# Performance work log

Hardware: AMD Instinct MI355X
Metric: run time of the kernel (lower is better)

## Reference

```python
import jax, jax.numpy as jnp
import numpy as np

K = 7            # involution kernel size
GC = 16          # group_channels (canonical involution)
EPS = 1e-6


def ln_cf(x, w, b):
    # channels_first LayerNorm over channel dim (axis=1), as in ConvNeXt utils
    u = jnp.mean(x, axis=1, keepdims=True)
    s = jnp.mean((x - u) ** 2, axis=1, keepdims=True)
    xn = (x - u) / jnp.sqrt(s + EPS)
    return w[:, None, None] * xn + b[:, None, None]


def gelu(x):
    return jax.nn.gelu(x, approximate=False)  # torch nn.GELU default (erf)


def involution(x, w1, b1, w2, b2):
    # x: (B,C,H,W). Kernel-generating head: 1x1 conv -> ReLU -> 1x1 conv.
    B, C, H, W = x.shape
    G = C // GC
    mid = jnp.einsum('bchw,mc->bmhw', x, w1) + b1[None, :, None, None]
    mid = jax.nn.relu(mid)
    wk = jnp.einsum('bmhw,km->bkhw', mid, w2) + b2[None, :, None, None]
    wk = wk.reshape(B, G, K * K, H, W)  # per-pixel, per-group K*K kernels
    pad = (K - 1) // 2
    xp = jnp.pad(x, ((0, 0), (0, 0), (pad, pad), (pad, pad)))
    out = jnp.zeros((B, G, GC, H, W), dtype=x.dtype)
    # accumulate over the K*K spatial offsets (fixed small loop, no big unfold)
    for idx in range(K * K):
        i, j = divmod(idx, K)
        xs = xp[:, :, i:i + H, j:j + W].reshape(B, G, GC, H, W)
        out = out + wk[:, :, idx][:, :, None] * xs
    return out.reshape(B, C, H, W)


def setup_inputs() -> dict:
    key = jax.random.key(0)
    ks = jax.random.split(key, 8)
    B, C, O, H, Wd = 4, 128, 256, 128, 128
    mid = C // 4
    G = C // GC
    sc = 0.05
    return {
        'x': jax.random.normal(ks[0], (B, C, H, Wd), jnp.float32),
        'w1': jax.random.normal(ks[1], (mid, C), jnp.float32) * sc,
        'b1': jnp.zeros((mid,), jnp.float32),
        'w2': jax.random.normal(ks[2], (K * K * G, mid), jnp.float32) * sc,
        'b2': jnp.zeros((K * K * G,), jnp.float32),
        'ln1_w': jnp.ones((C,), jnp.float32),
        'ln1_b': jnp.zeros((C,), jnp.float32),
        'conv_w': jax.random.normal(ks[3], (O, C), jnp.float32) * sc,
        'ln2_w': jnp.ones((O,), jnp.float32),
        'ln2_b': jnp.zeros((O,), jnp.float32),
        'map_w': jax.random.normal(ks[4], (O, C), jnp.float32) * sc,
        'map_b': jnp.zeros((O,), jnp.float32),
        'ln3_w': jnp.ones((O,), jnp.float32),
        'ln3_b': jnp.zeros((O,), jnp.float32),
    }


def reference(x, w1, b1, w2, b2, ln1_w, ln1_b, conv_w, ln2_w, ln2_b,
              map_w, map_b, ln3_w, ln3_b):
    # invblock: Involution -> LayerNorm(channels_first) -> GELU
    x1 = involution(x, w1, b1, w2, b2)
    x1 = gelu(ln_cf(x1, ln1_w, ln1_b))
    # conv_block: 1x1 conv (no bias) -> LayerNorm
    x1 = ln_cf(jnp.einsum('bchw,oc->bohw', x1, conv_w), ln2_w, ln2_b)
    # mapping (channels differ): 1x1 conv (bias) -> LayerNorm
    xm = jnp.einsum('bchw,oc->bohw', x, map_w) + map_b[None, :, None, None]
    xm = ln_cf(xm, ln3_w, ln3_b)
    return gelu(x1 + xm)
```

## Files before the change

kernel.cpp:

```cpp
#include <hip/hip_runtime.h>

typedef unsigned short ushort_t;
typedef unsigned int uint_t;

#define NB 4
#define NC 128
#define NH 128
#define NW 128
#define NPIX 65536
#define NMID 32
#define NKK 49
#define NK 392
#define NKP 400
#define NO 256
#define LN_EPS 1e-6f

typedef __attribute__((ext_vector_type(8))) short short8;
typedef __attribute__((ext_vector_type(4))) float floatx4;

__device__ __forceinline__ float bf2f(ushort_t u) {
    union { uint_t i; float f; } v; v.i = ((uint_t)u) << 16; return v.f;
}
__device__ __forceinline__ float bf2f_lo(uint_t u) {
    union { uint_t i; float f; } v; v.i = u << 16; return v.f;
}
__device__ __forceinline__ float bf2f_hi(uint_t u) {
    union { uint_t i; float f; } v; v.i = u & 0xffff0000u; return v.f;
}
__device__ __forceinline__ ushort_t f2bf(float f) {
    union { float f; uint_t i; } v; v.f = f;
    uint_t x = v.i;
    uint_t r = (x + 0x7FFFu + ((x >> 16) & 1u)) >> 16;
    return (ushort_t)r;
}
__device__ __forceinline__ float gelu_f(float x) {
    return 0.5f * x * (1.0f + erff(x * 0.70710678118654752f));
}
__device__ __forceinline__ float ldin(const void* p, int i, int isf32) {
    return isf32 ? ((const float*)p)[i] : bf2f(((const ushort_t*)p)[i]);
}
__device__ __forceinline__ void gload_lds16(const void* g, void* l) {
    __builtin_amdgcn_global_load_lds(
        (const __attribute__((address_space(1))) void*)g,
        (__attribute__((address_space(3))) void*)l, 16, 0, 0);
}

__global__ void kdetect(const uint_t* __restrict__ xw, int* __restrict__ flag) {
    int lane = threadIdx.x;
    int cnt = 0;
    for (int j = 0; j < 8; j++) {
        uint_t w = xw[lane * 8 + j];
        uint_t e = (w >> 7) & 0xffu;
        if (e >= 110u && e <= 135u) cnt++;
    }
    for (int d = 1; d < 64; d <<= 1) cnt += __shfl_xor(cnt, d);
    if (lane == 0) flag[0] = (cnt < 256) ? 1 : 0;
}

__global__ void ksentinel(uint_t* __restrict__ out, int nwords) {
    int i = blockIdx.x * 256 + threadIdx.x;
    if (i < nwords) out[i] = 0x40004000u;
}

__global__ __launch_bounds__(256) void ktrans(const void* __restrict__ x,
                                              ushort_t* __restrict__ xT,
                                              const int* __restrict__ flag) {
    int isf32 = flag[0];
    int b = blockIdx.z, h = blockIdx.y;
    int wchunk = blockIdx.x & 1, cchunk = blockIdx.x >> 1;
    int w0 = wchunk << 6, c0 = cchunk << 5;
    __shared__ ushort_t tile[32][66];
    int tx = threadIdx.x & 63, ty = threadIdx.x >> 6;
    for (int r = 0; r < 32; r += 4) {
        int idx = (((b * NC + c0 + r + ty) * NH) + h) * NW + w0 + tx;
        tile[r + ty][tx] = isf32 ? f2bf(((const float*)x)[idx])
                                 : ((const ushort_t*)x)[idx];
    }
    __syncthreads();
    int cc = threadIdx.x & 31, wq = threadIdx.x >> 5;
    for (int pp = 0; pp < 64; pp += 8) {
        int wx = pp + wq;
        xT[((size_t)((b * NH + h) * NW) + w0 + wx) * NC + c0 + cc] = tile[cc][wx];
    }
}

__global__ __launch_bounds__(256) void kprep(const void* w1, const void* w2,
                                             const void* b1, const void* b2,
                                             const void* ln1w, const void* ln1b,
                                             const void* ln2w, const void* ln2b,
                                             const void* map_b,
                                             const void* ln3w, const void* ln3b,
                                             const int* __restrict__ flag,
                                             ushort_t* __restrict__ w1b,
                                             ushort_t* __restrict__ w2b,
                                             float* __restrict__ b1f,
                                             float* __restrict__ b2f,
                                             float* __restrict__ ln1wf,
                                             float* __restrict__ ln1bf,
                                             float* __restrict__ ln2wf,
                                             float* __restrict__ ln2bf,
                                             float* __restrict__ mbf,
                                             float* __restrict__ ln3wf,
                                             float* __restrict__ ln3bf) {
    int isf32 = flag[0];
    int i = blockIdx.x * 256 + threadIdx.x;
    if (i < NMID * NC) w1b[i] = f2bf(ldin(w1, i, isf32));
    if (i < NKP * NMID) w2b[i] = (i < NK * NMID) ? f2bf(ldin(w2, i, isf32))
                                                 : (ushort_t)0;
    if (i < NMID) b1f[i] = ldin(b1, i, isf32);
    if (i < NKP)  b2f[i] = (i < NK) ? ldin(b2, i, isf32) : 0.f;
    if (i < NC) { ln1wf[i] = ldin(ln1w, i, isf32); ln1bf[i] = ldin(ln1b, i, isf32); }
    if (i < NO) {
        ln2wf[i] = ldin(ln2w, i, isf32); ln2bf[i] = ldin(ln2b, i, isf32);
        mbf[i]   = ldin(map_b, i, isf32);
        ln3wf[i] = ldin(ln3w, i, isf32); ln3bf[i] = ldin(ln3b, i, isf32);
    }
}

__global__ __launch_bounds__(256) void kfrag(const void* conv_w, const void* map_w,
                                             const int* __restrict__ flag,
                                             ushort_t* __restrict__ wfrag) {
    int isf32 = flag[0];
    int cid = blockIdx.x * 256 + threadIdx.x;
    int lane = cid & 63, n4 = (cid >> 6) & 15, br = (cid >> 10) & 1, kb = cid >> 11;
    int o = n4 * 16 + (lane & 15);
    int ch0 = kb * 32 + (lane >> 4) * 8;
    const void* src = br ? map_w : conv_w;
    ushort_t* dst = wfrag + (size_t)cid * 8;
#pragma unroll
    for (int j = 0; j < 8; j++)
        dst[j] = f2bf(ldin(src, o * NC + ch0 + j, isf32));
}

__global__ __launch_bounds__(256) void k1a(const ushort_t* __restrict__ xT,
                                           const ushort_t* __restrict__ w1b,
                                           const float* __restrict__ b1f,
                                           const ushort_t* __restrict__ w2b,
                                           const float* __restrict__ b2f,
                                           ushort_t* __restrict__ wkT) {
    __shared__ ushort_t midbuf[64 * 32];
    __shared__ ushort_t wkstage[NKP * 66];

    int t = threadIdx.x;
    int lane = t & 63;
    int w = __builtin_amdgcn_readfirstlane(t >> 6);
    int l16 = lane & 15, quad = lane >> 4;
    int tileid = blockIdx.x;
    int tilex = tileid & 15, tiley = (tileid >> 4) & 15, b = tileid >> 8;
    int h0 = tiley * 8, w0 = tilex * 8;

    int lpx_a = 16 * w + l16;
    int py = lpx_a >> 3, pxx = lpx_a & 7;
    const ushort_t* abase = xT + (size_t)((b * NH + h0 + py) * NW + w0 + pxx) * NC + quad * 8;
    floatx4 am0 = (floatx4)0.f, am1 = (floatx4)0.f;
#pragma unroll
    for (int kb = 0; kb < 4; kb++) {
        short8 a   = *(const short8*)(abase + kb * 32);
        short8 b0  = *(const short8*)(w1b + (l16) * NC + kb * 32 + quad * 8);
        short8 b1v = *(const short8*)(w1b + (16 + l16) * NC + kb * 32 + quad * 8);
        am0 = __builtin_amdgcn_mfma_f32_16x16x32_bf16(a, b0, am0, 0, 0, 0);
        am1 = __builtin_amdgcn_mfma_f32_16x16x32_bf16(a, b1v, am1, 0, 0, 0);
    }
    {
        float bia0 = b1f[l16], bia1 = b1f[16 + l16];
#pragma unroll
        for (int r = 0; r < 4; r++) {
            int m = 16 * w + quad * 4 + r;
            midbuf[m * 32 + l16]      = f2bf(fmaxf(am0[r] + bia0, 0.f));
            midbuf[m * 32 + 16 + l16] = f2bf(fmaxf(am1[r] + bia1, 0.f));
        }
    }
    __syncthreads();

    short8 aM = *(const short8*)(midbuf + (16 * w + l16) * 32 + quad * 8);
#pragma unroll
    for (int nt = 0; nt < 25; nt++) {
        int n = nt * 16 + l16;
        short8 bw = *(const short8*)(w2b + n * 32 + quad * 8);
        floatx4 c = __builtin_amdgcn_mfma_f32_16x16x32_bf16(aM, bw, (floatx4)0.f, 0, 0, 0);
        float bias = b2f[n];
#pragma unroll
        for (int r = 0; r < 4; r++)
            wkstage[n * 66 + 16 * w + quad * 4 + r] = f2bf(c[r] + bias);
    }
    __syncthreads();

    int krow = t >> 5, px2 = t & 31;
    for (int it = 0; it < 50; it++) {
        int k = it * 8 + krow;
        uint_t v = *(const uint_t*)&wkstage[k * 66 + 2 * px2];
        *(uint_t*)&wkT[(size_t)k * NPIX + tileid * 64 + 2 * px2] = v;
    }
}

__global__ __launch_bounds__(512) void k1b(const ushort_t* __restrict__ xT,
                                           const ushort_t* __restrict__ wkT,
                                           const float* __restrict__ ln1wf,
                                           const float* __restrict__ ln1bf,
                                           ushort_t* __restrict__ y1) {
    __shared__ __align__(16) char smem[50432];
    uint4* x8   = (uint4*)smem;
    float* sred = (float*)smem;

    int t = threadIdx.x;
    int lane = t & 63;
    int w = __builtin_amdgcn_readfirstlane(t >> 6);
    int tileid = blockIdx.x;
    int tilex = tileid & 15, tiley = (tileid >> 4) & 15, b = tileid >> 8;
    int h0 = tiley * 8, w0 = tilex * 8;
    int py = lane >> 3, pxx = lane & 7;

    const ushort_t* wkbase = wkT + (size_t)(w * NKK) * NPIX + tileid * 64 + lane;
    uint_t wkp[25];
#pragma unroll
    for (int j = 0; j < 24; j++) {
        uint_t lo = wkbase[(size_t)(2 * j) * NPIX];
        uint_t hi = wkbase[(size_t)(2 * j + 1) * NPIX];
        wkp[j] = lo | (hi << 16);
    }
    wkp[24] = wkbase[(size_t)48 * NPIX];

    for (int it = 0; it < 7; it++) {
        int idx = it * 512 + t;
        if (idx < 3136) {
            int oct = idx & 15, hp = idx >> 4;
            int hy = hp / 14, hx = hp - hy * 14;
            int gh = h0 + hy - 3, gw = w0 + hx - 3;
            uint4 v = make_uint4(0u, 0u, 0u, 0u);
            if ((unsigned)gh < (unsigned)NH && (unsigned)gw < (unsigned)NW) {
                v = *(const uint4*)&xT[(size_t)((b * NH + gh) * NW + gw) * NC + 8 * oct];
            }
            x8[oct * 197 + hp] = v;
        }
    }
    __syncthreads();

    int base0 = py * 14 + pxx;
    float a[16];
#pragma unroll
    for (int j = 0; j < 16; j++) a[j] = 0.f;

#pragma unroll
    for (int tap = 0; tap < NKK; tap++) {
        float wkf = (tap & 1) ? bf2f((ushort_t)(wkp[tap >> 1] >> 16))
                              : bf2f((ushort_t)(wkp[tap >> 1] & 0xffffu));
        int xa = base0 + (tap / 7) * 14 + (tap % 7);
        uint4 u0 = x8[(2 * w) * 197 + xa];
        uint4 u1 = x8[(2 * w + 1) * 197 + xa];
        a[0]  = fmaf(wkf, bf2f_lo(u0.x), a[0]);
        a[1]  = fmaf(wkf, bf2f_hi(u0.x), a[1]);
        a[2]  = fmaf(wkf, bf2f_lo(u0.y), a[2]);
        a[3]  = fmaf(wkf, bf2f_hi(u0.y), a[3]);
        a[4]  = fmaf(wkf, bf2f_lo(u0.z), a[4]);
        a[5]  = fmaf(wkf, bf2f_hi(u0.z), a[5]);
        a[6]  = fmaf(wkf, bf2f_lo(u0.w), a[6]);
        a[7]  = fmaf(wkf, bf2f_hi(u0.w), a[7]);
        a[8]  = fmaf(wkf, bf2f_lo(u1.x), a[8]);
        a[9]  = fmaf(wkf, bf2f_hi(u1.x), a[9]);
        a[10] = fmaf(wkf, bf2f_lo(u1.y), a[10]);
        a[11] = fmaf(wkf, bf2f_hi(u1.y), a[11]);
        a[12] = fmaf(wkf, bf2f_lo(u1.z), a[12]);
        a[13] = fmaf(wkf, bf2f_hi(u1.z), a[13]);
        a[14] = fmaf(wkf, bf2f_lo(u1.w), a[14]);
        a[15] = fmaf(wkf, bf2f_hi(u1.w), a[15]);
    }
    __syncthreads();

    float s = 0.f, sq = 0.f;
#pragma unroll
    for (int j = 0; j < 16; j++) { s += a[j]; sq += a[j] * a[j]; }
    sred[(w * 64 + lane) * 2]     = s;
    sred[(w * 64 + lane) * 2 + 1] = sq;
    __syncthreads();
    float ts = 0.f, tq = 0.f;
#pragma unroll
    for (int r = 0; r < 8; r++) {
        ts += sred[(r * 64 + lane) * 2];
        tq += sred[(r * 64 + lane) * 2 + 1];
    }
    float mean = ts * (1.0f / NC);
    float var = tq * (1.0f / NC) - mean * mean;
    float rstd = rsqrtf(var + LN_EPS);

    int p = (b * NH + h0 + py) * NW + w0 + pxx;
    uint_t pk[8];
#pragma unroll
    for (int j = 0; j < 8; j++) {
        int c0 = 16 * w + 2 * j;
        float g0 = gelu_f((a[2 * j] - mean) * rstd * ln1wf[c0] + ln1bf[c0]);
        float g1 = gelu_f((a[2 * j + 1] - mean) * rstd * ln1wf[c0 + 1] + ln1bf[c0 + 1]);
        pk[j] = (uint_t)f2bf(g0) | ((uint_t)f2bf(g1) << 16);
    }
    uint4* dst = (uint4*)(y1 + (size_t)p * NC + 16 * w);
    dst[0] = make_uint4(pk[0], pk[1], pk[2], pk[3]);
    dst[1] = make_uint4(pk[4], pk[5], pk[6], pk[7]);
}

__global__ __launch_bounds__(64) void k1_fused(const ushort_t* __restrict__ xT,
                                               const ushort_t* __restrict__ w1b,
                                               const float* __restrict__ b1f,
                                               const ushort_t* __restrict__ w2b,
                                               const float* __restrict__ b2f,
                                               const float* __restrict__ ln1wf,
                                               const float* __restrict__ ln1bf,
                                               ushort_t* __restrict__ y1) {
    __shared__ ushort_t midbuf[16 * 32];
    __shared__ ushort_t wkbuf[16 * NKP];

    int lane = threadIdx.x;
    int l16 = lane & 15, quad = lane >> 4;
    int b = blockIdx.z;
    int h0 = blockIdx.y * 2, w0 = blockIdx.x * 8;

    int Pa = (b * NH + h0 + (l16 >> 3)) * NW + w0 + (l16 & 7);
    const ushort_t* abase = xT + (size_t)Pa * NC + quad * 8;
    floatx4 am0 = (floatx4)0.f, am1 = (floatx4)0.f;
#pragma unroll
    for (int kb = 0; kb < 4; kb++) {
        short8 a   = *(const short8*)(abase + kb * 32);
        short8 b0  = *(const short8*)(w1b + (l16) * NC + kb * 32 + quad * 8);
        short8 b1v = *(const short8*)(w1b + (16 + l16) * NC + kb * 32 + quad * 8);
        am0 = __builtin_amdgcn_mfma_f32_16x16x32_bf16(a, b0, am0, 0, 0, 0);
        am1 = __builtin_amdgcn_mfma_f32_16x16x32_bf16(a, b1v, am1, 0, 0, 0);
    }
    {
        float bia0 = b1f[l16], bia1 = b1f[16 + l16];
#pragma unroll
        for (int r = 0; r < 4; r++) {
            int m = quad * 4 + r;
            midbuf[m * 32 + l16]      = f2bf(fmaxf(am0[r] + bia0, 0.f));
            midbuf[m * 32 + 16 + l16] = f2bf(fmaxf(am1[r] + bia1, 0.f));
        }
    }
    __syncthreads();

    short8 aM = *(const short8*)(midbuf + l16 * 32 + quad * 8);
#pragma unroll
    for (int nt = 0; nt < 25; nt++) {
        int n = nt * 16 + l16;
        short8 bw = *(const short8*)(w2b + n * 32 + quad * 8);
        floatx4 c = __builtin_amdgcn_mfma_f32_16x16x32_bf16(aM, bw, (floatx4)0.f, 0, 0, 0);
        float bias = b2f[n];
#pragma unroll
        for (int r = 0; r < 4; r++)
            wkbuf[(quad * 4 + r) * NKP + n] = f2bf(c[r] + bias);
    }
    __syncthreads();

    int g = lane >> 3;
    float l1w0 = ln1wf[2 * lane], l1w1 = ln1wf[2 * lane + 1];
    float l1b0 = ln1bf[2 * lane], l1b1 = ln1bf[2 * lane + 1];

    for (int i = 0; i < 16; i++) {
        int hh0 = h0 + (i >> 3), ww0 = w0 + (i & 7);
        int p = (b * NH + hh0) * NW + ww0;
        const ushort_t* wkrow = wkbuf + i * NKP + g * NKK;
        float a0 = 0.f, a1 = 0.f;
#pragma unroll
        for (int dy = -3; dy <= 3; dy++) {
            int hh = hh0 + dy;
            if ((unsigned)hh >= (unsigned)NH) continue;
#pragma unroll
            for (int dx = -3; dx <= 3; dx++) {
                int ww = ww0 + dx;
                if ((unsigned)ww >= (unsigned)NW) continue;
                float wkv = bf2f(wkrow[(dy + 3) * 7 + (dx + 3)]);
                uint_t xp = *(const uint_t*)(xT + ((size_t)(p + dy * NW + dx)) * NC + 2 * lane);
                a0 = fmaf(wkv, bf2f((ushort_t)(xp & 0xffffu)), a0);
                a1 = fmaf(wkv, bf2f((ushort_t)(xp >> 16)), a1);
            }
        }
        float s = a0 + a1, sq = a0 * a0 + a1 * a1;
#pragma unroll
        for (int d = 1; d < 64; d <<= 1) {
            s  += __shfl_xor(s, d);
            sq += __shfl_xor(sq, d);
        }
        float mean = s * (1.0f / NC);
        float var = sq * (1.0f / NC) - mean * mean;
        float rstd = rsqrtf(var + LN_EPS);
        float g0 = gelu_f((a0 - mean) * rstd * l1w0 + l1b0);
        float g1 = gelu_f((a1 - mean) * rstd * l1w1 + l1b1);
        uint_t pk = (uint_t)f2bf(g0) | ((uint_t)f2bf(g1) << 16);
        *(uint_t*)(y1 + (size_t)p * NC + 2 * lane) = pk;
    }
}

__global__ __launch_bounds__(256, 4) void k23(const ushort_t* __restrict__ y1,
                                              const ushort_t* __restrict__ xT,
                                              const ushort_t* __restrict__ wfrag,
                                              const float* __restrict__ mbf,
                                              const float* __restrict__ ln2wf,
                                              const float* __restrict__ ln2bf,
                                              const float* __restrict__ ln3wf,
                                              const float* __restrict__ ln3bf,
                                              void* __restrict__ out,
                                              const int* __restrict__ flag) {
    __shared__ __align__(16) char sbuf[32768];

    int isf32 = flag[0];
    int t = threadIdx.x;
    int lane = t & 63;
    int w = __builtin_amdgcn_readfirstlane(t >> 6);
    int quad = lane >> 4, l16 = lane & 15;
    int pair = w >> 1;
    int oh   = w & 1;

    int P0 = blockIdx.x * 32;
    int pw = P0 + pair * 16;
    const ushort_t* aYp = y1 + (size_t)(pw + l16) * NC + quad * 8;
    const ushort_t* aXp = xT + (size_t)(pw + l16) * NC + quad * 8;

    {
        const ushort_t* gsrc = wfrag + (size_t)(w * 512 + lane) * 8;
        char* ldst = sbuf + (size_t)(w * 512) * 16;
#pragma unroll
        for (int i = 0; i < 8; i++)
            gload_lds16(gsrc + i * 64 * 8, ldst + i * 64 * 16);
    }
    short8 Ay[4], Ax[4];
#pragma unroll
    for (int kb = 0; kb < 4; kb++) {
        Ay[kb] = *(const short8*)(aYp + kb * 32);
        Ax[kb] = *(const short8*)(aXp + kb * 32);
    }
    __syncthreads();

    floatx4 accC[8], accM[8];
#pragma unroll
    for (int j = 0; j < 8; j++) { accC[j] = (floatx4)0.f; accM[j] = (floatx4)0.f; }

#pragma unroll
    for (int kb = 0; kb < 4; kb++) {
        short8 ay = Ay[kb], ax = Ax[kb];
#pragma unroll
        for (int j = 0; j < 8; j++) {
            int n4 = oh * 8 + j;
            short8 bc = *(const short8*)(sbuf + (size_t)(n4 * 64 + lane) * 16);
            short8 bm = *(const short8*)(sbuf + 16384 + (size_t)(n4 * 64 + lane) * 16);
            accC[j] = __builtin_amdgcn_mfma_f32_16x16x32_bf16(ay, bc, accC[j], 0, 0, 0);
            accM[j] = __builtin_amdgcn_mfma_f32_16x16x32_bf16(ax, bm, accM[j], 0, 0, 0);
        }
        __syncthreads();
        if (kb < 3) {
            const ushort_t* gsrc = wfrag + ((size_t)(kb + 1) * 2048 + w * 512 + lane) * 8;
            char* ldst = sbuf + (size_t)(w * 512) * 16;
#pragma unroll
            for (int i = 0; i < 8; i++)
                gload_lds16(gsrc + i * 64 * 8, ldst + i * 64 * 16);
            __syncthreads();
        }
    }

#pragma unroll
    for (int j = 0; j < 8; j++) {
        float mb = mbf[(oh * 8 + j) * 16 + l16];
#pragma unroll
        for (int r = 0; r < 4; r++) accM[j][r] += mb;
    }

    floatx4 s1 = (floatx4)0.f, q1 = (floatx4)0.f, s2 = (floatx4)0.f, q2 = (floatx4)0.f;
#pragma unroll
    for (int j = 0; j < 8; j++)
#pragma unroll
        for (int r = 0; r < 4; r++) {
            float a = accC[j][r], m = accM[j][r];
            s1[r] += a; q1[r] += a * a;
            s2[r] += m; q2[r] += m * m;
        }
#pragma unroll
    for (int d = 1; d < 16; d <<= 1) {
#pragma unroll
        for (int r = 0; r < 4; r++) {
            s1[r] += __shfl_xor(s1[r], d);
            q1[r] += __shfl_xor(q1[r], d);
            s2[r] += __shfl_xor(s2[r], d);
            q2[r] += __shfl_xor(q2[r], d);
        }
    }

    float* sstat = (float*)sbuf;
    if (l16 == 0) {
#pragma unroll
        for (int r = 0; r < 4; r++) {
            float* sp = sstat + (((pair * 2 + oh) * 16) + quad * 4 + r) * 4;
            sp[0] = s1[r]; sp[1] = q1[r]; sp[2] = s2[r]; sp[3] = q2[r];
        }
    }
    __syncthreads();

    floatx4 mn1, rs1, mn2, rs2;
#pragma unroll
    for (int r = 0; r < 4; r++) {
        const float* op = sstat + (((pair * 2 + (oh ^ 1)) * 16) + quad * 4 + r) * 4;
        float S1 = s1[r] + op[0], Q1 = q1[r] + op[1];
        float S2 = s2[r] + op[2], Q2 = q2[r] + op[3];
        mn1[r] = S1 * (1.0f / NO);
        rs1[r] = rsqrtf(Q1 * (1.0f / NO) - mn1[r] * mn1[r] + LN_EPS);
        mn2[r] = S2 * (1.0f / NO);
        rs2[r] = rsqrtf(Q2 * (1.0f / NO) - mn2[r] * mn2[r] + LN_EPS);
    }

    int batch = pw >> 14;
    int plocal = (pw & 16383) + quad * 4;
#pragma unroll
    for (int j = 0; j < 8; j++) {
        int o = (oh * 8 + j) * 16 + l16;
        float l2w = ln2wf[o], l2b = ln2bf[o];
        float l3w = ln3wf[o], l3b = ln3bf[o];
        float4 gv;
        {
            float v1, v2;
            v1 = (accC[j][0] - mn1[0]) * rs1[0] * l2w + l2b;
            v2 = (accM[j][0] - mn2[0]) * rs2[0] * l3w + l3b;
            gv.x = gelu_f(v1 + v2);
            v1 = (accC[j][1] - mn1[1]) * rs1[1] * l2w + l2b;
            v2 = (accM[j][1] - mn2[1]) * rs2[1] * l3w + l3b;
            gv.y = gelu_f(v1 + v2);
            v1 = (accC[j][2] - mn1[2]) * rs1[2] * l2w + l2b;
            v2 = (accM[j][2] - mn2[2]) * rs2[2] * l3w + l3b;
            gv.z = gelu_f(v1 + v2);
            v1 = (accC[j][3] - mn1[3]) * rs1[3] * l2w + l2b;
            v2 = (accM[j][3] - mn2[3]) * rs2[3] * l3w + l3b;
            gv.w = gelu_f(v1 + v2);
        }
        size_t oi = ((size_t)(batch * NO + o) << 14) + plocal;
        if (isf32) {
            *(float4*)((float*)out + oi) = gv;
        } else {
            uint_t p0 = (uint_t)f2bf(gv.x) | ((uint_t)f2bf(gv.y) << 16);
            uint_t p1 = (uint_t)f2bf(gv.z) | ((uint_t)f2bf(gv.w) << 16);
            *(uint2*)((ushort_t*)out + oi) = make_uint2(p0, p1);
        }
    }
}

extern "C" void kernel_launch(void* const* d_in, const int* in_sizes, int n_in,
                              void* d_out, int out_size, void* d_ws, size_t ws_size,
                              hipStream_t stream) {
    const void* x      = d_in[0];
    const void* w1     = d_in[1];
    const void* b1     = d_in[2];
    const void* w2     = d_in[3];
    const void* b2     = d_in[4];
    const void* ln1w   = d_in[5];
    const void* ln1b   = d_in[6];
    const void* conv_w = d_in[7];
    const void* ln2w   = d_in[8];
    const void* ln2b   = d_in[9];
    const void* map_w  = d_in[10];
    const void* map_b  = d_in[11];
    const void* ln3w   = d_in[12];
    const void* ln3b   = d_in[13];

    char* ws = (char*)d_ws;
    ushort_t* xT    = (ushort_t*)(ws);
    ushort_t* y1    = (ushort_t*)(ws + 16777216);
    ushort_t* wfrag = (ushort_t*)(ws + 33554432);
    ushort_t* w1b   = (ushort_t*)(ws + 33685504);
    ushort_t* w2b   = (ushort_t*)(ws + 33693696);
    float*    b1f   = (float*)(ws + 33719296);
    float*    b2f   = (float*)(ws + 33719424);
    float*    ln1wf = (float*)(ws + 33721024);
    float*    ln1bf = (float*)(ws + 33721536);
    float*    mbf   = (float*)(ws + 33722048);
    float*    ln2wf = (float*)(ws + 33723072);
    float*    ln2bf = (float*)(ws + 33724096);
    float*    ln3wf = (float*)(ws + 33725120);
    float*    ln3bf = (float*)(ws + 33726144);
    int*      flag  = (int*)(ws + 33727168);
    const size_t NEED_SMALL = 33727184;
    ushort_t* wkT   = (ushort_t*)(ws + 33727232);
    const size_t NEED_BIG = 33727232 + (size_t)NKP * NPIX * 2;

    if (ws_size < NEED_SMALL) {
        int nwords = out_size / 2;
        ksentinel<<<(nwords + 255) / 256, 256, 0, stream>>>((uint_t*)d_out, nwords);
        return;
    }

    kdetect<<<1, 64, 0, stream>>>((const uint_t*)x, flag);
    kprep<<<128, 256, 0, stream>>>(w1, w2, b1, b2, ln1w, ln1b,
                                   ln2w, ln2b, map_b, ln3w, ln3b, flag,
                                   w1b, w2b, b1f, b2f, ln1wf, ln1bf,
                                   ln2wf, ln2bf, mbf, ln3wf, ln3bf);
    kfrag<<<32, 256, 0, stream>>>(conv_w, map_w, flag, wfrag);
    ktrans<<<dim3(8, 128, 4), 256, 0, stream>>>(x, xT, flag);

    if (ws_size >= NEED_BIG) {
        k1a<<<1024, 256, 0, stream>>>(xT, w1b, b1f, w2b, b2f, wkT);
        k1b<<<1024, 512, 0, stream>>>(xT, wkT, ln1wf, ln1bf, y1);
    } else {
        k1_fused<<<dim3(16, 64, 4), 64, 0, stream>>>(xT, w1b, b1f, w2b, b2f,
                                                     ln1wf, ln1bf, y1);
    }

    k23<<<NPIX / 32, 256, 0, stream>>>(y1, xT, wfrag, mbf,
                                       ln2wf, ln2bf, ln3wf, ln3bf, d_out, flag);
}
```

Baseline: 222.9 us.

## Fuse kernel generation and involution into one kernel, merge prep launches

Merges the per-pixel kernel-generating head (k1a) and the involution+LayerNorm+GELU stage (k1b) into a single 512-thread kernel that keeps the generated 7x7 weights in shared memory. This removes the large wkT round trip through global memory. The weight-prep and fragment-packing kernels are also combined into one launch. The involution now reads x neighbours straight from global memory instead of from a staged shared-memory halo, so it relies on cache reuse, and the channel reduction uses an 8-lane shuffle.

New measurement: 223.5 us. Within noise of the previous version (+0.3%).

```diff
diff --git a/kernel.cpp b/kernel.cpp
--- a/kernel.cpp
+++ b/kernel.cpp
@@ -84,60 +84,62 @@
     }
 }
 
-__global__ __launch_bounds__(256) void kprep(const void* w1, const void* w2,
-                                             const void* b1, const void* b2,
-                                             const void* ln1w, const void* ln1b,
-                                             const void* ln2w, const void* ln2b,
-                                             const void* map_b,
-                                             const void* ln3w, const void* ln3b,
-                                             const int* __restrict__ flag,
-                                             ushort_t* __restrict__ w1b,
-                                             ushort_t* __restrict__ w2b,
-                                             float* __restrict__ b1f,
-                                             float* __restrict__ b2f,
-                                             float* __restrict__ ln1wf,
-                                             float* __restrict__ ln1bf,
-                                             float* __restrict__ ln2wf,
-                                             float* __restrict__ ln2bf,
-                                             float* __restrict__ mbf,
-                                             float* __restrict__ ln3wf,
-                                             float* __restrict__ ln3bf) {
+__global__ __launch_bounds__(256) void kprepfrag(const void* w1, const void* w2,
+                                                 const void* b1, const void* b2,
+                                                 const void* ln1w, const void* ln1b,
+                                                 const void* ln2w, const void* ln2b,
+                                                 const void* map_b,
+                                                 const void* ln3w, const void* ln3b,
+                                                 const void* conv_w, const void* map_w,
+                                                 const int* __restrict__ flag,
+                                                 ushort_t* __restrict__ w1b,
+                                                 ushort_t* __restrict__ w2b,
+                                                 float* __restrict__ b1f,
+                                                 float* __restrict__ b2f,
+                                                 float* __restrict__ ln1wf,
+                                                 float* __restrict__ ln1bf,
+                                                 float* __restrict__ ln2wf,
+                                                 float* __restrict__ ln2bf,
+                                                 float* __restrict__ mbf,
+                                                 float* __restrict__ ln3wf,
+                                                 float* __restrict__ ln3bf,
+                                                 ushort_t* __restrict__ wfrag) {
     int isf32 = flag[0];
-    int i = blockIdx.x * 256 + threadIdx.x;
-    if (i < NMID * NC) w1b[i] = f2bf(ldin(w1, i, isf32));
-    if (i < NKP * NMID) w2b[i] = (i < NK * NMID) ? f2bf(ldin(w2, i, isf32))
-                                                 : (ushort_t)0;
-    if (i < NMID) b1f[i] = ldin(b1, i, isf32);
-    if (i < NKP)  b2f[i] = (i < NK) ? ldin(b2, i, isf32) : 0.f;
-    if (i < NC) { ln1wf[i] = ldin(ln1w, i, isf32); ln1bf[i] = ldin(ln1b, i, isf32); }
-    if (i < NO) {
-        ln2wf[i] = ldin(ln2w, i, isf32); ln2bf[i] = ldin(ln2b, i, isf32);
-        mbf[i]   = ldin(map_b, i, isf32);
-        ln3wf[i] = ldin(ln3w, i, isf32); ln3bf[i] = ldin(ln3b, i, isf32);
-    }
-}
-
-__global__ __launch_bounds__(256) void kfrag(const void* conv_w, const void* map_w,
-                                             const int* __restrict__ flag,
-                                             ushort_t* __restrict__ wfrag) {
-    int isf32 = flag[0];
-    int cid = blockIdx.x * 256 + threadIdx.x;
-    int lane = cid & 63, n4 = (cid >> 6) & 15, br = (cid >> 10) & 1, kb = cid >> 11;
-    int o = n4 * 16 + (lane & 15);
-    int ch0 = kb * 32 + (lane >> 4) * 8;
-    const void* src = br ? map_w : conv_w;
-    ushort_t* dst = wfrag + (size_t)cid * 8;
-#pragma unroll
-    for (int j = 0; j < 8; j++)
-        dst[j] = f2bf(ldin(src, o * NC + ch0 + j, isf32));
-}
-
-__global__ __launch_bounds__(256) void k1a(const ushort_t* __restrict__ xT,
+    int bid = blockIdx.x;
+    if (bid < 128) {
+        int i = bid * 256 + threadIdx.x;
+        if (i < NMID * NC) w1b[i] = f2bf(ldin(w1, i, isf32));
+        if (i < NKP * NMID) w2b[i] = (i < NK * NMID) ? f2bf(ldin(w2, i, isf32))
+                                                     : (ushort_t)0;
+        if (i < NMID) b1f[i] = ldin(b1, i, isf32);
+        if (i < NKP)  b2f[i] = (i < NK) ? ldin(b2, i, isf32) : 0.f;
+        if (i < NC) { ln1wf[i] = ldin(ln1w, i, isf32); ln1bf[i] = ldin(ln1b, i, isf32); }
+        if (i < NO) {
+            ln2wf[i] = ldin(ln2w, i, isf32); ln2bf[i] = ldin(ln2b, i, isf32);
+            mbf[i]   = ldin(map_b, i, isf32);
+            ln3wf[i] = ldin(ln3w, i, isf32); ln3bf[i] = ldin(ln3b, i, isf32);
+        }
+    } else {
+        int cid = (bid - 128) * 256 + threadIdx.x;
+        int lane = cid & 63, n4 = (cid >> 6) & 15, br = (cid >> 10) & 1, kb = cid >> 11;
+        int o = n4 * 16 + (lane & 15);
+        int ch0 = kb * 32 + (lane >> 4) * 8;
+        const void* src = br ? map_w : conv_w;
+        ushort_t* dst = wfrag + (size_t)cid * 8;
+#pragma unroll
+        for (int j = 0; j < 8; j++)
+            dst[j] = f2bf(ldin(src, o * NC + ch0 + j, isf32));
+    }
+}
+
+__global__ __launch_bounds__(512) void k1f(const ushort_t* __restrict__ xT,
                                            const ushort_t* __restrict__ w1b,
                                            const float* __restrict__ b1f,
                                            const ushort_t* __restrict__ w2b,
                                            const float* __restrict__ b2f,
-                                           ushort_t* __restrict__ wkT) {
+                                           const float* __restrict__ ln1wf,
+                                           const float* __restrict__ ln1bf,
+                                           ushort_t* __restrict__ y1) {
     __shared__ ushort_t midbuf[64 * 32];
     __shared__ ushort_t wkstage[NKP * 66];
 
@@ -148,20 +150,21 @@
     int tileid = blockIdx.x;
     int tilex = tileid & 15, tiley = (tileid >> 4) & 15, b = tileid >> 8;
     int h0 = tiley * 8, w0 = tilex * 8;
-
-    int lpx_a = 16 * w + l16;
-    int py = lpx_a >> 3, pxx = lpx_a & 7;
-    const ushort_t* abase = xT + (size_t)((b * NH + h0 + py) * NW + w0 + pxx) * NC + quad * 8;
-    floatx4 am0 = (floatx4)0.f, am1 = (floatx4)0.f;
-#pragma unroll
-    for (int kb = 0; kb < 4; kb++) {
-        short8 a   = *(const short8*)(abase + kb * 32);
-        short8 b0  = *(const short8*)(w1b + (l16) * NC + kb * 32 + quad * 8);
-        short8 b1v = *(const short8*)(w1b + (16 + l16) * NC + kb * 32 + quad * 8);
-        am0 = __builtin_amdgcn_mfma_f32_16x16x32_bf16(a, b0, am0, 0, 0, 0);
-        am1 = __builtin_amdgcn_mfma_f32_16x16x32_bf16(a, b1v, am1, 0, 0, 0);
-    }
-    {
+    int w4 = w & 3;
+
+    if (w < 4) {
+        int lpx = 16 * w + l16;
+        int py = lpx >> 3, pxx = lpx & 7;
+        const ushort_t* abase = xT + (size_t)((b * NH + h0 + py) * NW + w0 + pxx) * NC + quad * 8;
+        floatx4 am0 = (floatx4)0.f, am1 = (floatx4)0.f;
+#pragma unroll
+        for (int kb = 0; kb < 4; kb++) {
+            short8 a   = *(const short8*)(abase + kb * 32);
+            short8 b0  = *(const short8*)(w1b + (l16) * NC + kb * 32 + quad * 8);
+            short8 b1v = *(const short8*)(w1b + (16 + l16) * NC + kb * 32 + quad * 8);
+            am0 = __builtin_amdgcn_mfma_f32_16x16x32_bf16(a, b0, am0, 0, 0, 0);
+            am1 = __builtin_amdgcn_mfma_f32_16x16x32_bf16(a, b1v, am1, 0, 0, 0);
+        }
         float bia0 = b1f[l16], bia1 = b1f[16 + l16];
 #pragma unroll
         for (int r = 0; r < 4; r++) {
@@ -172,218 +175,86 @@
     }
     __syncthreads();
 
-    short8 aM = *(const short8*)(midbuf + (16 * w + l16) * 32 + quad * 8);
-#pragma unroll
-    for (int nt = 0; nt < 25; nt++) {
-        int n = nt * 16 + l16;
-        short8 bw = *(const short8*)(w2b + n * 32 + quad * 8);
-        floatx4 c = __builtin_amdgcn_mfma_f32_16x16x32_bf16(aM, bw, (floatx4)0.f, 0, 0, 0);
-        float bias = b2f[n];
-#pragma unroll
-        for (int r = 0; r < 4; r++)
-            wkstage[n * 66 + 16 * w + quad * 4 + r] = f2bf(c[r] + bias);
+    {
+        short8 aM = *(const short8*)(midbuf + (16 * w4 + l16) * 32 + quad * 8);
+        int nt0 = (w < 4) ? 0 : 13;
+        int nt1 = (w < 4) ? 13 : 25;
+        for (int nt = nt0; nt < nt1; nt++) {
+            int n = nt * 16 + l16;
+            short8 bw = *(const short8*)(w2b + n * 32 + quad * 8);
+            floatx4 c = __builtin_amdgcn_mfma_f32_16x16x32_bf16(aM, bw, (floatx4)0.f, 0, 0, 0);
+            float bias = b2f[n];
+#pragma unroll
+            for (int r = 0; r < 4; r++)
+                wkstage[n * 66 + 16 * w4 + quad * 4 + r] = f2bf(c[r] + bias);
+        }
     }
     __syncthreads();
 
-    int krow = t >> 5, px2 = t & 31;
-    for (int it = 0; it < 50; it++) {
-        int k = it * 8 + krow;
-        uint_t v = *(const uint_t*)&wkstage[k * 66 + 2 * px2];
-        *(uint_t*)&wkT[(size_t)k * NPIX + tileid * 64 + 2 * px2] = v;
-    }
-}
-
-__global__ __launch_bounds__(512) void k1b(const ushort_t* __restrict__ xT,
-                                           const ushort_t* __restrict__ wkT,
-                                           const float* __restrict__ ln1wf,
-                                           const float* __restrict__ ln1bf,
-                                           ushort_t* __restrict__ y1) {
-    __shared__ __align__(16) char smem[50432];
-    uint4* x8   = (uint4*)smem;
-    float* sred = (float*)smem;
-
-    int t = threadIdx.x;
-    int lane = t & 63;
-    int w = __builtin_amdgcn_readfirstlane(t >> 6);
-    int tileid = blockIdx.x;
-    int tilex = tileid & 15, tiley = (tileid >> 4) & 15, b = tileid >> 8;
-    int h0 = tiley * 8, w0 = tilex * 8;
-    int py = lane >> 3, pxx = lane & 7;
-
-    const ushort_t* wkbase = wkT + (size_t)(w * NKK) * NPIX + tileid * 64 + lane;
-    uint_t wkp[25];
-#pragma unroll
-    for (int j = 0; j < 24; j++) {
-        uint_t lo = wkbase[(size_t)(2 * j) * NPIX];
-        uint_t hi = wkbase[(size_t)(2 * j + 1) * NPIX];
-        wkp[j] = lo | (hi << 16);
-    }
-    wkp[24] = wkbase[(size_t)48 * NPIX];
-
-    for (int it = 0; it < 7; it++) {
-        int idx = it * 512 + t;
-        if (idx < 3136) {
-            int oct = idx & 15, hp = idx >> 4;
-            int hy = hp / 14, hx = hp - hy * 14;
-            int gh = h0 + hy - 3, gw = w0 + hx - 3;
-            uint4 v = make_uint4(0u, 0u, 0u, 0u);
-            if ((unsigned)gh < (unsigned)NH && (unsigned)gw < (unsigned)NW) {
-                v = *(const uint4*)&xT[(size_t)((b * NH + gh) * NW + gw) * NC + 8 * oct];
-            }
-            x8[oct * 197 + hp] = v;
-        }
-    }
-    __syncthreads();
-
-    int base0 = py * 14 + pxx;
+    int px = t >> 3, g = t & 7;
+    int hy = px >> 3, hx = px & 7;
+    int hh0 = h0 + hy, ww0 = w0 + hx;
+    int p = (b * NH + hh0) * NW + ww0;
+    const ushort_t* wkcol = wkstage + px;
+
     float a[16];
 #pragma unroll
     for (int j = 0; j < 16; j++) a[j] = 0.f;
 
 #pragma unroll
-    for (int tap = 0; tap < NKK; tap++) {
-        float wkf = (tap & 1) ? bf2f((ushort_t)(wkp[tap >> 1] >> 16))
-                              : bf2f((ushort_t)(wkp[tap >> 1] & 0xffffu));
-        int xa = base0 + (tap / 7) * 14 + (tap % 7);
-        uint4 u0 = x8[(2 * w) * 197 + xa];
-        uint4 u1 = x8[(2 * w + 1) * 197 + xa];
-        a[0]  = fmaf(wkf, bf2f_lo(u0.x), a[0]);
-        a[1]  = fmaf(wkf, bf2f_hi(u0.x), a[1]);
-        a[2]  = fmaf(wkf, bf2f_lo(u0.y), a[2]);
-        a[3]  = fmaf(wkf, bf2f_hi(u0.y), a[3]);
-        a[4]  = fmaf(wkf, bf2f_lo(u0.z), a[4]);
-        a[5]  = fmaf(wkf, bf2f_hi(u0.z), a[5]);
-        a[6]  = fmaf(wkf, bf2f_lo(u0.w), a[6]);
-        a[7]  = fmaf(wkf, bf2f_hi(u0.w), a[7]);
-        a[8]  = fmaf(wkf, bf2f_lo(u1.x), a[8]);
-        a[9]  = fmaf(wkf, bf2f_hi(u1.x), a[9]);
-        a[10] = fmaf(wkf, bf2f_lo(u1.y), a[10]);
-        a[11] = fmaf(wkf, bf2f_hi(u1.y), a[11]);
-        a[12] = fmaf(wkf, bf2f_lo(u1.z), a[12]);
-        a[13] = fmaf(wkf, bf2f_hi(u1.z), a[13]);
-        a[14] = fmaf(wkf, bf2f_lo(u1.w), a[14]);
-        a[15] = fmaf(wkf, bf2f_hi(u1.w), a[15]);
-    }
-    __syncthreads();
+    for (int dy = -3; dy <= 3; dy++) {
+        int hh = hh0 + dy;
+        if ((unsigned)hh >= (unsigned)NH) continue;
+#pragma unroll
+        for (int dx = -3; dx <= 3; dx++) {
+            int ww = ww0 + dx;
+            if ((unsigned)ww >= (unsigned)NW) continue;
+            int tap = (dy + 3) * 7 + (dx + 3);
+            float wkv = bf2f(wkcol[(g * NKK + tap) * 66]);
+            const uint4* xq = (const uint4*)(xT + (size_t)(p + dy * NW + dx) * NC + g * 16);
+            uint4 u0 = xq[0], u1 = xq[1];
+            a[0]  = fmaf(wkv, bf2f_lo(u0.x), a[0]);
+            a[1]  = fmaf(wkv, bf2f_hi(u0.x), a[1]);
+            a[2]  = fmaf(wkv, bf2f_lo(u0.y), a[2]);
+            a[3]  = fmaf(wkv, bf2f_hi(u0.y), a[3]);
+            a[4]  = fmaf(wkv, bf2f_lo(u0.z), a[4]);
+            a[5]  = fmaf(wkv, bf2f_hi(u0.z), a[5]);
+            a[6]  = fmaf(wkv, bf2f_lo(u0.w), a[6]);
+            a[7]  = fmaf(wkv, bf2f_hi(u0.w), a[7]);
+            a[8]  = fmaf(wkv, bf2f_lo(u1.x), a[8]);
+            a[9]  = fmaf(wkv, bf2f_hi(u1.x), a[9]);
+            a[10] = fmaf(wkv, bf2f_lo(u1.y), a[10]);
+            a[11] = fmaf(wkv, bf2f_hi(u1.y), a[11]);
+            a[12] = fmaf(wkv, bf2f_lo(u1.z), a[12]);
+            a[13] = fmaf(wkv, bf2f_hi(u1.z), a[13]);
+            a[14] = fmaf(wkv, bf2f_lo(u1.w), a[14]);
+            a[15] = fmaf(wkv, bf2f_hi(u1.w), a[15]);
+        }
+    }
 
     float s = 0.f, sq = 0.f;
 #pragma unroll
     for (int j = 0; j < 16; j++) { s += a[j]; sq += a[j] * a[j]; }
-    sred[(w * 64 + lane) * 2]     = s;
-    sred[(w * 64 + lane) * 2 + 1] = sq;
-    __syncthreads();
-    float ts = 0.f, tq = 0.f;
-#pragma unroll
-    for (int r = 0; r < 8; r++) {
-        ts += sred[(r * 64 + lane) * 2];
-        tq += sred[(r * 64 + lane) * 2 + 1];
-    }
-    float mean = ts * (1.0f / NC);
-    float var = tq * (1.0f / NC) - mean * mean;
+#pragma unroll
+    for (int d = 1; d < 8; d <<= 1) {
+        s  += __shfl_xor(s, d);
+        sq += __shfl_xor(sq, d);
+    }
+    float mean = s * (1.0f / NC);
+    float var = sq * (1.0f / NC) - mean * mean;
     float rstd = rsqrtf(var + LN_EPS);
 
-    int p = (b * NH + h0 + py) * NW + w0 + pxx;
     uint_t pk[8];
 #pragma unroll
     for (int j = 0; j < 8; j++) {
-        int c0 = 16 * w + 2 * j;
+        int c0 = g * 16 + 2 * j;
         float g0 = gelu_f((a[2 * j] - mean) * rstd * ln1wf[c0] + ln1bf[c0]);
         float g1 = gelu_f((a[2 * j + 1] - mean) * rstd * ln1wf[c0 + 1] + ln1bf[c0 + 1]);
         pk[j] = (uint_t)f2bf(g0) | ((uint_t)f2bf(g1) << 16);
     }
-    uint4* dst = (uint4*)(y1 + (size_t)p * NC + 16 * w);
+    uint4* dst = (uint4*)(y1 + (size_t)p * NC + g * 16);
     dst[0] = make_uint4(pk[0], pk[1], pk[2], pk[3]);
     dst[1] = make_uint4(pk[4], pk[5], pk[6], pk[7]);
-}
-
-__global__ __launch_bounds__(64) void k1_fused(const ushort_t* __restrict__ xT,
-                                               const ushort_t* __restrict__ w1b,
-                                               const float* __restrict__ b1f,
-                                               const ushort_t* __restrict__ w2b,
-                                               const float* __restrict__ b2f,
-                                               const float* __restrict__ ln1wf,
-                                               const float* __restrict__ ln1bf,
-                                               ushort_t* __restrict__ y1) {
-    __shared__ ushort_t midbuf[16 * 32];
-    __shared__ ushort_t wkbuf[16 * NKP];
-
-    int lane = threadIdx.x;
-    int l16 = lane & 15, quad = lane >> 4;
-    int b = blockIdx.z;
-    int h0 = blockIdx.y * 2, w0 = blockIdx.x * 8;
-
-    int Pa = (b * NH + h0 + (l16 >> 3)) * NW + w0 + (l16 & 7);
-    const ushort_t* abase = xT + (size_t)Pa * NC + quad * 8;
-    floatx4 am0 = (floatx4)0.f, am1 = (floatx4)0.f;
-#pragma unroll
-    for (int kb = 0; kb < 4; kb++) {
-        short8 a   = *(const short8*)(abase + kb * 32);
-        short8 b0  = *(const short8*)(w1b + (l16) * NC + kb * 32 + quad * 8);
-        short8 b1v = *(const short8*)(w1b + (16 + l16) * NC + kb * 32 + quad * 8);
-        am0 = __builtin_amdgcn_mfma_f32_16x16x32_bf16(a, b0, am0, 0, 0, 0);
-        am1 = __builtin_amdgcn_mfma_f32_16x16x32_bf16(a, b1v, am1, 0, 0, 0);
-    }
-    {
-        float bia0 = b1f[l16], bia1 = b1f[16 + l16];
-#pragma unroll
-        for (int r = 0; r < 4; r++) {
-            int m = quad * 4 + r;
-            midbuf[m * 32 + l16]      = f2bf(fmaxf(am0[r] + bia0, 0.f));
-            midbuf[m * 32 + 16 + l16] = f2bf(fmaxf(am1[r] + bia1, 0.f));
-        }
-    }
-    __syncthreads();
-
-    short8 aM = *(const short8*)(midbuf + l16 * 32 + quad * 8);
-#pragma unroll
-    for (int nt = 0; nt < 25; nt++) {
-        int n = nt * 16 + l16;
-        short8 bw = *(const short8*)(w2b + n * 32 + quad * 8);
-        floatx4 c = __builtin_amdgcn_mfma_f32_16x16x32_bf16(aM, bw, (floatx4)0.f, 0, 0, 0);
-        float bias = b2f[n];
-#pragma unroll
-        for (int r = 0; r < 4; r++)
-            wkbuf[(quad * 4 + r) * NKP + n] = f2bf(c[r] + bias);
-    }
-    __syncthreads();
-
-    int g = lane >> 3;
-    float l1w0 = ln1wf[2 * lane], l1w1 = ln1wf[2 * lane + 1];
-    float l1b0 = ln1bf[2 * lane], l1b1 = ln1bf[2 * lane + 1];
-
-    for (int i = 0; i < 16; i++) {
-        int hh0 = h0 + (i >> 3), ww0 = w0 + (i & 7);
-        int p = (b * NH + hh0) * NW + ww0;
-        const ushort_t* wkrow = wkbuf + i * NKP + g * NKK;
-        float a0 = 0.f, a1 = 0.f;
-#pragma unroll
-        for (int dy = -3; dy <= 3; dy++) {
-            int hh = hh0 + dy;
-            if ((unsigned)hh >= (unsigned)NH) continue;
-#pragma unroll
-            for (int dx = -3; dx <= 3; dx++) {
-                int ww = ww0 + dx;
-                if ((unsigned)ww >= (unsigned)NW) continue;
-                float wkv = bf2f(wkrow[(dy + 3) * 7 + (dx + 3)]);
-                uint_t xp = *(const uint_t*)(xT + ((size_t)(p + dy * NW + dx)) * NC + 2 * lane);
-                a0 = fmaf(wkv, bf2f((ushort_t)(xp & 0xffffu)), a0);
-                a1 = fmaf(wkv, bf2f((ushort_t)(xp >> 16)), a1);
-            }
-        }
-        float s = a0 + a1, sq = a0 * a0 + a1 * a1;
-#pragma unroll
-        for (int d = 1; d < 64; d <<= 1) {
-            s  += __shfl_xor(s, d);
-            sq += __shfl_xor(sq, d);
-        }
-        float mean = s * (1.0f / NC);
-        float var = sq * (1.0f / NC) - mean * mean;
-        float rstd = rsqrtf(var + LN_EPS);
-        float g0 = gelu_f((a0 - mean) * rstd * l1w0 + l1b0);
-        float g1 = gelu_f((a1 - mean) * rstd * l1w1 + l1b1);
-        uint_t pk = (uint_t)f2bf(g0) | ((uint_t)f2bf(g1) << 16);
-        *(uint_t*)(y1 + (size_t)p * NC + 2 * lane) = pk;
-    }
 }
 
 __global__ __launch_bounds__(256, 4) void k23(const ushort_t* __restrict__ y1,
@@ -570,8 +441,6 @@
     float*    ln3bf = (float*)(ws + 33726144);
     int*      flag  = (int*)(ws + 33727168);
     const size_t NEED_SMALL = 33727184;
-    ushort_t* wkT   = (ushort_t*)(ws + 33727232);
-    const size_t NEED_BIG = 33727232 + (size_t)NKP * NPIX * 2;
 
     if (ws_size < NEED_SMALL) {
         int nwords = out_size / 2;
@@ -580,21 +449,13 @@
     }
 
     kdetect<<<1, 64, 0, stream>>>((const uint_t*)x, flag);
-    kprep<<<128, 256, 0, stream>>>(w1, w2, b1, b2, ln1w, ln1b,
-                                   ln2w, ln2b, map_b, ln3w, ln3b, flag,
-                                   w1b, w2b, b1f, b2f, ln1wf, ln1bf,
-                                   ln2wf, ln2bf, mbf, ln3wf, ln3bf);
-    kfrag<<<32, 256, 0, stream>>>(conv_w, map_w, flag, wfrag);
+    kprepfrag<<<160, 256, 0, stream>>>(w1, w2, b1, b2, ln1w, ln1b,
+                                       ln2w, ln2b, map_b, ln3w, ln3b,
+                                       conv_w, map_w, flag,
+                                       w1b, w2b, b1f, b2f, ln1wf, ln1bf,
+                                       ln2wf, ln2bf, mbf, ln3wf, ln3bf, wfrag);
     ktrans<<<dim3(8, 128, 4), 256, 0, stream>>>(x, xT, flag);
-
-    if (ws_size >= NEED_BIG) {
-        k1a<<<1024, 256, 0, stream>>>(xT, w1b, b1f, w2b, b2f, wkT);
-        k1b<<<1024, 512, 0, stream>>>(xT, wkT, ln1wf, ln1bf, y1);
-    } else {
-        k1_fused<<<dim3(16, 64, 4), 64, 0, stream>>>(xT, w1b, b1f, w2b, b2f,
-                                                     ln1wf, ln1bf, y1);
-    }
-
+    k1f<<<1024, 512, 0, stream>>>(xT, w1b, b1f, w2b, b2f, ln1wf, ln1bf, y1);
     k23<<<NPIX / 32, 256, 0, stream>>>(y1, xT, wfrag, mbf,
                                        ln2wf, ln2bf, ln3wf, ln3bf, d_out, flag);
 }
```
